# Optimization experiments

Hardware: AMD Instinct MI355X
Metric: run time of the kernel (lower is better)

Reference implementation:

```python
import jax, jax.numpy as jnp
import numpy as np

DIM, FFN, GC, NSET, K = 48, 2, 2, 32, 3
HID = DIM * FFN          # 96 hidden features
G = HID // GC            # 48 groups in KBA
CG = HID // G            # 2 channels per group
INTERC = 24              # min(dim, 24)
B, H, W = 4, 128, 128


def _conv(x, w, b=None, groups=1, pad=0):
    out = jax.lax.conv_general_dilated(
        x, w, (1, 1), [(pad, pad), (pad, pad)],
        dimension_numbers=('NCHW', 'OIHW', 'NCHW'),
        feature_group_count=groups)
    if b is not None:
        out = out + b[None, :, None, None]
    return out


def _kba(x, att, k, g, bb, ww):
    # x: [B,c,H,W], att: [B,nset,H,W], bb: [1,nset,c], ww: [1,nset,c*c//g*k*k]
    Bz, c, Hh, Ww = x.shape
    KK = k * k
    cg = c // g
    P = Hh * Ww
    a = att.reshape(Bz, -1, P).transpose(0, 2, 1)                     # [B,P,nset]
    bias = jnp.einsum('bpn,nc->bpc', a, bb[0])                        # [B,P,c]
    attk = jnp.einsum('bpn,nm->bpm', a, ww[0]).reshape(Bz, P, g, cg, cg * KK)
    pd = k // 2
    xp = jnp.pad(x, ((0, 0), (0, 0), (pd, pd), (pd, pd)))
    # im2col patches, torch.unfold layout: channel-major, kernel row-major
    patches = jnp.stack([xp[:, :, i:i + Hh, j:j + Ww]
                         for i in range(k) for j in range(k)], axis=2)  # [B,c,KK,H,W]
    uf = patches.reshape(Bz, g, cg * KK, P).transpose(0, 3, 1, 2)       # [B,P,g,cg*KK]
    out = jnp.einsum('bpgom,bpgm->bpgo', attk, uf).reshape(Bz, P, c) + bias
    return out.transpose(0, 2, 1).reshape(Bz, c, Hh, Ww)


def setup_inputs() -> dict:
    key = jax.random.key(0)
    ks = jax.random.split(key, 20)
    s = 0.05
    inp = {
        'x': jax.random.normal(ks[0], (B, DIM, H, W), jnp.float32),
        'dw1_w': jax.random.normal(ks[1], (HID, DIM, 1, 1), jnp.float32) * s,
        'dw2_w': jax.random.normal(ks[2], (HID, 1, 3, 3), jnp.float32) * s,
        'proj_w': jax.random.normal(ks[3], (DIM, HID, 1, 1), jnp.float32) * s,
        'sca_w': jax.random.normal(ks[4], (HID, HID, 1, 1), jnp.float32) * s,
        'sca_b': jax.random.normal(ks[5], (HID,), jnp.float32) * s,
        'c1_w1': jax.random.normal(ks[6], (HID, DIM, 1, 1), jnp.float32) * s,
        'c1_w2': jax.random.normal(ks[7], (HID, 1, 3, 3), jnp.float32) * s,
        'kba_w': jax.random.normal(ks[8], (1, NSET, HID * CG * K * K), jnp.float32) * s,
        'kba_b': jax.random.normal(ks[9], (1, NSET, HID), jnp.float32) * s,
        'c2_w1': jax.random.normal(ks[10], (INTERC, DIM // INTERC, 3, 3), jnp.float32) * s,
        'c2_b1': jax.random.normal(ks[11], (INTERC,), jnp.float32) * s,
        'c2_w2': jax.random.normal(ks[12], (NSET, INTERC // 2, 1, 1), jnp.float32) * s,
        'c2_b2': jax.random.normal(ks[13], (NSET,), jnp.float32) * s,
        'c211_w': jax.random.normal(ks[14], (NSET, DIM, 1, 1), jnp.float32) * s,
        'c211_b': jax.random.normal(ks[15], (NSET,), jnp.float32) * s,
        'attgamma': jnp.full((1, NSET, 1, 1), 0.01, jnp.float32),
        'ga1': jnp.full((1, HID, 1, 1), 0.01, jnp.float32),
    }
    return inp


def reference(x, dw1_w, dw2_w, proj_w, sca_w, sca_b, c1_w1, c1_w2,
              kba_w, kba_b, c2_w1, c2_b1, c2_w2, c2_b2,
              c211_w, c211_b, attgamma, ga1):
    # dwconv branch: 1x1 -> depthwise 3x3
    x1 = _conv(_conv(x, dw1_w), dw2_w, groups=HID, pad=1)
    # attention map branch: grouped 3x3 -> SimpleGate -> 1x1, scaled + skip 1x1
    t = _conv(x, c2_w1, c2_b1, groups=INTERC, pad=1)
    t1, t2 = jnp.split(t, 2, axis=1)
    t = _conv(t1 * t2, c2_w2, c2_b2)
    att = t * attgamma + _conv(x, c211_w, c211_b)
    # conv1 branch feeding KBA
    uf = _conv(_conv(x, c1_w1), c1_w2, groups=HID, pad=1)
    x2 = _kba(uf, att, K, G, kba_b, kba_w) * ga1 + uf
    comb = jax.nn.gelu(x1, approximate=False) * x2
    pooled = jnp.mean(comb, axis=(2, 3), keepdims=True)
    comb = comb * _conv(pooled, sca_w, sca_b)
    return _conv(comb, proj_w)
```

## Files before the change

### kernel.cpp

```cpp
#include <hip/hip_runtime.h>
#include <math.h>

#define BB 4
#define HH 128
#define WW 128
#define HWP (HH*WW)
#define DIMC 48
#define HIDC 96
#define NSETC 32

#define XS_W 27
#define HS_W 102
#define US_W 102

typedef __attribute__((ext_vector_type(8))) short bf16x8;
typedef __attribute__((ext_vector_type(4))) float f32x4;
typedef __attribute__((ext_vector_type(2))) float f32x2;

static __device__ __forceinline__ unsigned short f2bf(float f) {
    union { float f; unsigned u; } v; v.f = f;
    unsigned r = (v.u + 0x7FFFu + ((v.u >> 16) & 1u)) >> 16;
    return (unsigned short)r;
}
static __device__ __forceinline__ unsigned rnd_bf(float f) {
    union { float f; unsigned u; } v; v.f = f;
    return v.u + 0x8000u;
}
static __device__ __forceinline__ unsigned pack2bf(float lo, float hi) {
    return __builtin_amdgcn_perm(rnd_bf(hi), rnd_bf(lo), 0x07060302u);
}
static __device__ __forceinline__ void st_bf_hi(unsigned short* p, float f) {
    *p = (unsigned short)(rnd_bf(f) >> 16);
}
static __device__ __forceinline__ float bf2f(unsigned short u) {
    union { unsigned u; float f; } v; v.u = ((unsigned)u) << 16;
    return v.f;
}
static __device__ __forceinline__ float bfpair_lo(unsigned pr) {
    union { unsigned u; float f; } v; v.u = pr << 16; return v.f;
}
static __device__ __forceinline__ float bfpair_hi(unsigned pr) {
    union { unsigned u; float f; } v; v.u = pr & 0xffff0000u; return v.f;
}
static __device__ __forceinline__ float gelu(float x) {
    return 0.5f * x * (1.0f + erff(x * 0.70710678118654752f));
}

__global__ __launch_bounds__(256) void k_prep(
    const float* __restrict__ x,
    const float* __restrict__ kbaw, const float* __restrict__ kbab,
    const float* __restrict__ dw1w, const float* __restrict__ c1w1,
    const float* __restrict__ ga1,  const float* __restrict__ c211w,
    const float* __restrict__ c2w2, const float* __restrict__ c2b2,
    const float* __restrict__ c211b, const float* __restrict__ attg,
    unsigned short* __restrict__ Bpk, unsigned short* __restrict__ Bpw,
    unsigned short* __restrict__ Aps, unsigned short* __restrict__ Ag,
    unsigned* __restrict__ x_p, float* __restrict__ pooled)
{
    __shared__ unsigned ts[256 * 26];
    int blk = blockIdx.x, tid = threadIdx.x;
    if (blk < 300) {
        int t = blk * 256 + tid;
        if (t < 61440) {
            int j = t & 7, lane = (t >> 3) & 63, tile = t >> 9;
            int chunk = tile / 10, nt = tile - chunk * 10;
            int m = lane & 15, qn = lane >> 4;
            int lc = 4 * nt + (m & 3);
            int o = lc / 20, tt = lc % 20;
            int c = (m >> 2) * 24 + 2 * chunk + o;
            int n = qn * 8 + j;
            float v = 0.f;
            if (tt < 18)       v = kbaw[n * 1728 + (c >> 1) * 36 + (c & 1) * 18 + tt] * ga1[c];
            else if (tt == 18) v = kbab[n * 96 + c] * ga1[c];
            Bpk[t] = f2bf(v);
        } else if (t < 73728) {
            int u = t - 61440;
            int s = u / 6144;
            int rem = u % 6144;
            int nt = rem >> 9;
            int lane = (rem >> 3) & 63, j = rem & 7;
            int k = s * 32 + ((lane >> 4) << 3) + j;
            int col = (nt << 4) + (lane & 15);
            float v = 0.f;
            if (k < 48) v = (col < 96) ? dw1w[col * 48 + k] : c1w1[(col - 96) * 48 + k];
            Bpw[u] = f2bf(v);
        } else if (t < 75776) {
            int u = t - 73728;
            int j = u & 7, lane = (u >> 3) & 63, tile = u >> 9;
            int kt = tile >> 1, nt2 = tile & 1;
            int m = lane & 15, qn = lane >> 4;
            int n = 8 * (m >> 2) + 4 * nt2 + (m & 3);
            int k = kt * 32 + qn * 8 + j;
            Aps[u] = f2bf(k < 48 ? c211w[n * 48 + k] : 0.f);
        } else if (t < 76800) {
            int u = t - 75776;
            int j = u & 7, lane = (u >> 3) & 63, nt2 = u >> 9;
            int m = lane & 15, qn = lane >> 4;
            int n = 8 * (m >> 2) + 4 * nt2 + (m & 3);
            int k = qn * 8 + j;
            float v = 0.f;
            if (k < 12)       v = c2w2[n * 12 + k] * attg[n];
            else if (k == 12) v = c2b2[n] * attg[n] + c211b[n];
            Ag[u] = f2bf(v);
        }
    } else {
        int xblk = blk - 300;
        if (xblk == 0) {
            for (int i = tid; i < BB * HIDC; i += 256) pooled[i] = 0.f;
        }
        int b = xblk >> 6;
        int p0 = (xblk & 63) << 8;
        const float* xb = x + (size_t)b * DIMC * HWP + p0;
        #pragma unroll
        for (int c2 = 0; c2 < 24; ++c2) {
            float lo = xb[(2 * c2) * HWP + tid];
            float hi = xb[(2 * c2 + 1) * HWP + tid];
            ts[tid * 26 + c2] = pack2bf(lo, hi);
        }
        __syncthreads();
        unsigned* dst = x_p + ((size_t)b * HWP + p0) * 24;
        for (int idx = tid; idx < 256 * 24; idx += 256) {
            int px = idx / 24, j2 = idx - px * 24;
            dst[px * 24 + j2] = ts[px * 26 + j2];
        }
    }
}

__global__ __launch_bounds__(512, 4) void k_mff(
    const unsigned* __restrict__ x_p,
    const uint4* __restrict__ BpkA, const uint4* __restrict__ Bpw,
    const uint4* __restrict__ Aps,  const uint4* __restrict__ Ag,
    const float* __restrict__ c1w2, const float* __restrict__ dw2w,
    const float* __restrict__ c2w1, const float* __restrict__ c2b1,
    unsigned* __restrict__ comb_bf, float* __restrict__ pooled)
{
    __shared__ __attribute__((aligned(16))) unsigned xs[144 * XS_W];
    __shared__ __attribute__((aligned(16))) unsigned short hsw[144 * HS_W];
    __shared__ unsigned short us2p[100 * US_W];
    __shared__ float wls[864 + 432 + 24];
    __shared__ float pooled_s[96];

    int lane = threadIdx.x, wy = threadIdx.y;
    int tid = wy * 64 + lane;
    int blk = blockIdx.x;
    int b = blk >> 8, ty = (blk >> 4) & 15, tx = blk & 15;
    int q = lane >> 4, i16 = lane & 15;
    int wh = wy >> 2;
    int wp = wy & 3;

    float* wats  = wls + 864;
    float* c2b1s = wls + 864 + 432;
    float* att_tf = (float*)hsw;

    if (tid < 96) pooled_s[tid] = 0.f;
    for (int idx = tid; idx < 864; idx += 512) {
        int t5 = idx / 96, c = idx - t5 * 96;
        wls[idx] = dw2w[c * 9 + t5];
    }
    for (int idx = tid; idx < 216; idx += 512) {
        int g = idx / 9, tap = idx - g * 9;
        wats[idx * 2]     = c2w1[g * 18 + tap];
        wats[idx * 2 + 1] = c2w1[g * 18 + 9 + tap];
    }
    if (tid < 24) c2b1s[tid] = c2b1[tid];
    for (int idx = tid; idx < 144 * 12; idx += 512) {
        int pos = idx / 12, jp = idx - pos * 12;
        int gy = ty * 8 - 2 + pos / 12, gx = tx * 8 - 2 + pos % 12;
        uint2 v = {0u, 0u};
        if (((unsigned)gy < (unsigned)HH) & ((unsigned)gx < (unsigned)WW))
            v = *(const uint2*)&x_p[((size_t)b * HWP + gy * WW + gx) * 24 + jp * 2];
        xs[pos * XS_W + jp * 2]     = v.x;
        xs[pos * XS_W + jp * 2 + 1] = v.y;
    }
    __syncthreads();

    int p_t = wp * 16 + i16;
    int pyT = p_t >> 3, pxT = p_t & 7;
    int gp = (ty * 8 + pyT) * WW + tx * 8 + pxT;
    uint4 z4 = {0u, 0u, 0u, 0u};

    #pragma unroll
    for (int ci = 0; ci < 3; ++ci) {
        int g = q * 6 + wh * 3 + ci;
        float acc = c2b1s[g];
        #pragma unroll
        for (int di = 0; di < 3; ++di)
          #pragma unroll
          for (int dj = 0; dj < 3; ++dj) {
              unsigned pr = xs[((pyT + 1 + di) * 12 + pxT + 1 + dj) * XS_W + g];
              f32x2 w2 = *(const f32x2*)&wats[(g * 9 + di * 3 + dj) * 2];
              acc += w2.x * bfpair_lo(pr) + w2.y * bfpair_hi(pr);
          }
        att_tf[p_t * XS_W + g] = acc;
    }
    __syncthreads();

    bf16x8 afrag;
    {
        int p26 = p_t * XS_W;
        unsigned tgd[4];
        #pragma unroll
        for (int i2 = 0; i2 < 4; ++i2) {
            int k0 = q * 8 + 2 * i2;
            int k1 = k0 + 1;
            float v0 = (k0 < 12) ? att_tf[p26 + k0] * att_tf[p26 + 12 + k0] : (k0 == 12 ? 1.f : 0.f);
            float v1 = (k1 < 12) ? att_tf[p26 + k1] * att_tf[p26 + 12 + k1] : (k1 == 12 ? 1.f : 0.f);
            tgd[i2] = pack2bf(v0, v1);
        }
        uint4 tgr = {tgd[0], tgd[1], tgd[2], tgd[3]};
        bf16x8 btg = __builtin_bit_cast(bf16x8, tgr);

        int cen = (pyT + 2) * 12 + (pxT + 2);
        int cb = cen * XS_W + q * 4;
        uint4 bx0r = {xs[cb], xs[cb + 1], xs[cb + 2], xs[cb + 3]};
        uint4 bx1r = z4;
        if (q < 2) {
            int cb2 = cen * XS_W + 16 + q * 4;
            bx1r.x = xs[cb2]; bx1r.y = xs[cb2 + 1]; bx1r.z = xs[cb2 + 2]; bx1r.w = xs[cb2 + 3];
        }
        bf16x8 bx0 = __builtin_bit_cast(bf16x8, bx0r);
        bf16x8 bx1 = __builtin_bit_cast(bf16x8, bx1r);

        float attv[8];
        #pragma unroll
        for (int nt2 = 0; nt2 < 2; ++nt2) {
            bf16x8 ag  = __builtin_bit_cast(bf16x8, Ag[nt2 * 64 + lane]);
            bf16x8 as0 = __builtin_bit_cast(bf16x8, Aps[nt2 * 64 + lane]);
            bf16x8 as1 = __builtin_bit_cast(bf16x8, Aps[(2 + nt2) * 64 + lane]);
            f32x4 z = {0.f, 0.f, 0.f, 0.f};
            f32x4 c = __builtin_amdgcn_mfma_f32_16x16x32_bf16(ag, btg, z, 0, 0, 0);
            c = __builtin_amdgcn_mfma_f32_16x16x32_bf16(as1, bx1, c, 0, 0, 0);
            c = __builtin_amdgcn_mfma_f32_16x16x32_bf16(as0, bx0, c, 0, 0, 0);
            #pragma unroll
            for (int r = 0; r < 4; ++r) attv[nt2 * 4 + r] = c[r];
        }
        uint4 au = {pack2bf(attv[0], attv[1]), pack2bf(attv[2], attv[3]),
                    pack2bf(attv[4], attv[5]), pack2bf(attv[6], attv[7])};
        afrag = __builtin_bit_cast(bf16x8, au);
    }
    __syncthreads();

    {
        {
            int rg = wy;
            int hp = rg * 16 + i16;
            int ab = hp * XS_W + q * 4;
            uint4 a0r = {xs[ab], xs[ab + 1], xs[ab + 2], xs[ab + 3]};
            uint4 a1r = z4;
            if (q < 2) {
                int ab2 = hp * XS_W + 16 + q * 4;
                a1r.x = xs[ab2]; a1r.y = xs[ab2 + 1]; a1r.z = xs[ab2 + 2]; a1r.w = xs[ab2 + 3];
            }
            bf16x8 a0 = __builtin_bit_cast(bf16x8, a0r);
            bf16x8 a1 = __builtin_bit_cast(bf16x8, a1r);
            int rowb = rg * 16 + 4 * q;
            #pragma unroll
            for (int nt = 0; nt < 6; ++nt) {
                bf16x8 b0 = __builtin_bit_cast(bf16x8, Bpw[(size_t)((6 + nt) << 6) + lane]);
                bf16x8 b1 = __builtin_bit_cast(bf16x8, Bpw[(size_t)((18 + nt) << 6) + lane]);
                f32x4 z = {0.f, 0.f, 0.f, 0.f};
                f32x4 c = __builtin_amdgcn_mfma_f32_16x16x32_bf16(a1, b1, z, 0, 0, 0);
                c = __builtin_amdgcn_mfma_f32_16x16x32_bf16(a0, b0, c, 0, 0, 0);
                #pragma unroll
                for (int r = 0; r < 4; ++r)
                    st_bf_hi(&hsw[(rowb + r) * HS_W + nt * 16 + i16], c[r]);
            }
        }
        if (wy >= 1 && wy <= 6) {
            int hp = 128 + i16;
            int ab = hp * XS_W + q * 4;
            uint4 a0r = {xs[ab], xs[ab + 1], xs[ab + 2], xs[ab + 3]};
            uint4 a1r = z4;
            if (q < 2) {
                int ab2 = hp * XS_W + 16 + q * 4;
                a1r.x = xs[ab2]; a1r.y = xs[ab2 + 1]; a1r.z = xs[ab2 + 2]; a1r.w = xs[ab2 + 3];
            }
            bf16x8 a0 = __builtin_bit_cast(bf16x8, a0r);
            bf16x8 a1 = __builtin_bit_cast(bf16x8, a1r);
            int rowb = 128 + 4 * q;
            int nt = wy - 1;
            bf16x8 b0 = __builtin_bit_cast(bf16x8, Bpw[(size_t)((6 + nt) << 6) + lane]);
            bf16x8 b1 = __builtin_bit_cast(bf16x8, Bpw[(size_t)((18 + nt) << 6) + lane]);
            f32x4 z = {0.f, 0.f, 0.f, 0.f};
            f32x4 c = __builtin_amdgcn_mfma_f32_16x16x32_bf16(a1, b1, z, 0, 0, 0);
            c = __builtin_amdgcn_mfma_f32_16x16x32_bf16(a0, b0, c, 0, 0, 0);
            #pragma unroll
            for (int r = 0; r < 4; ++r)
                st_bf_hi(&hsw[(rowb + r) * HS_W + nt * 16 + i16], c[r]);
        }
    }
    __syncthreads();

    #pragma unroll 1
    for (int it = 0; it < 3; ++it) {
        int su = wy * 3 + it;
        int cq = su >> 1;
        const float* w9 = c1w2 + cq * 8 * 9;
        int hp2 = (su & 1) * 50 + lane;
        if (lane < 50) {
            int py2 = hp2 / 10, px2 = hp2 - py2 * 10;
            float acc[8];
            #pragma unroll
            for (int c = 0; c < 8; ++c) acc[c] = 0.f;
            #pragma unroll
            for (int di = 0; di < 3; ++di)
              #pragma unroll
              for (int dj = 0; dj < 3; ++dj) {
                  int rb = ((py2 + di) * 12 + px2 + dj) * HS_W + cq * 8;
                  unsigned pp[4];
                  pp[0] = *(const unsigned*)&hsw[rb];
                  pp[1] = *(const unsigned*)&hsw[rb + 2];
                  pp[2] = *(const unsigned*)&hsw[rb + 4];
                  pp[3] = *(const unsigned*)&hsw[rb + 6];
                  #pragma unroll
                  for (int c2 = 0; c2 < 4; ++c2) {
                      acc[2*c2]   += w9[(2*c2) * 9 + di * 3 + dj]   * bfpair_lo(pp[c2]);
                      acc[2*c2+1] += w9[(2*c2+1) * 9 + di * 3 + dj] * bfpair_hi(pp[c2]);
                  }
              }
            int wb = hp2 * US_W + cq * 8;
            *(unsigned*)&us2p[wb]     = pack2bf(acc[0], acc[1]);
            *(unsigned*)&us2p[wb + 2] = pack2bf(acc[2], acc[3]);
            *(unsigned*)&us2p[wb + 4] = pack2bf(acc[4], acc[5]);
            *(unsigned*)&us2p[wb + 6] = pack2bf(acc[6], acc[7]);
        }
    }
    __syncthreads();

    if (wy < 7) {
        int rg = wy;
        int hp = rg * 16 + i16;
        bool okp = hp < 100;
        int hy = hp / 10, hx = hp - hy * 10;
        int pos = okp ? ((hy + 1) * 12 + hx + 1) : 0;
        int ab = pos * XS_W + q * 4;
        uint4 a0r = {xs[ab], xs[ab + 1], xs[ab + 2], xs[ab + 3]};
        uint4 a1r = z4;
        if (q < 2) {
            int ab2 = pos * XS_W + 16 + q * 4;
            a1r.x = xs[ab2]; a1r.y = xs[ab2 + 1]; a1r.z = xs[ab2 + 2]; a1r.w = xs[ab2 + 3];
        }
        bf16x8 a0 = __builtin_bit_cast(bf16x8, a0r);
        bf16x8 a1 = __builtin_bit_cast(bf16x8, a1r);
        int rowb = rg * 16 + 4 * q;
        #pragma unroll
        for (int nt = 0; nt < 6; ++nt) {
            bf16x8 b0 = __builtin_bit_cast(bf16x8, Bpw[(size_t)(nt << 6) + lane]);
            bf16x8 b1 = __builtin_bit_cast(bf16x8, Bpw[(size_t)((12 + nt) << 6) + lane]);
            f32x4 z = {0.f, 0.f, 0.f, 0.f};
            f32x4 c = __builtin_amdgcn_mfma_f32_16x16x32_bf16(a1, b1, z, 0, 0, 0);
            c = __builtin_amdgcn_mfma_f32_16x16x32_bf16(a0, b0, c, 0, 0, 0);
            #pragma unroll
            for (int r = 0; r < 4; ++r)
                st_bf_hi(&hsw[(rowb + r) * HS_W + nt * 16 + i16], c[r]);
        }
    }
    __syncthreads();

    f32x2 greg[6];
    {
        int base = q * 24 + wh * 12;
        #pragma unroll
        for (int cc = 0; cc < 6; ++cc) {
            int c0 = base + 2 * cc;
            f32x2 acc = {0.f, 0.f};
            #pragma unroll
            for (int di = 0; di < 3; ++di)
              #pragma unroll
              for (int dj = 0; dj < 3; ++dj) {
                  unsigned pr = *(const unsigned*)&hsw[((pyT + di) * 10 + pxT + dj) * HS_W + c0];
                  f32x2 hv = {bfpair_lo(pr), bfpair_hi(pr)};
                  f32x2 wv = *(const f32x2*)&wls[(di * 3 + dj) * 96 + c0];
                  acc += wv * hv;
              }
            greg[cc].x = gelu(acc.x);
            greg[cc].y = gelu(acc.y);
        }
    }

    unsigned* cmb = comb_bf + ((size_t)b * HWP + gp) * 48 + q * 12;
    int hpC = (pyT + 1) * 10 + pxT + 1;
    const uint4* bpk_base = BpkA + (size_t)(wh * 60) * 64 + lane;

    uint4 buf[2][10];
    #pragma unroll
    for (int nt = 0; nt < 10; ++nt) buf[0][nt] = bpk_base[(size_t)nt << 6];

    #pragma unroll
    for (int cl = 0; cl < 6; ++cl) {
        int chunk = wh * 6 + cl;
        if (cl < 5) {
            #pragma unroll
            for (int nt = 0; nt < 10; ++nt)
                buf[(cl + 1) & 1][nt] = bpk_base[(size_t)(((cl + 1) * 10 + nt)) << 6];
        }
        int c0 = q * 24 + 2 * chunk;
        float u[18];
        #pragma unroll
        for (int i = 0; i < 3; ++i)
          #pragma unroll
          for (int j = 0; j < 3; ++j) {
              unsigned pr = *(const unsigned*)&us2p[((pyT + i) * 10 + pxT + j) * US_W + c0];
              u[i * 3 + j]     = bfpair_lo(pr);
              u[9 + i * 3 + j] = bfpair_hi(pr);
          }
        unsigned sp = *(const unsigned*)&us2p[hpC * US_W + c0];
        f32x4 cf[10];
        #pragma unroll
        for (int nt = 0; nt < 10; ++nt) {
            bf16x8 aW = __builtin_bit_cast(bf16x8, buf[cl & 1][nt]);
            f32x4 z = {0.f, 0.f, 0.f, 0.f};
            cf[nt] = __builtin_amdgcn_mfma_f32_16x16x32_bf16(aW, afrag, z, 0, 0, 0);
        }
        float acc0 = cf[4][2];
        float acc1 = cf[9][2];
        #pragma unroll
        for (int m = 0; m < 16; ++m) {
            acc0 += cf[m >> 2][m & 3]       * u[m];
            acc1 += cf[5 + (m >> 2)][m & 3] * u[m];
        }
        acc0 += cf[4][0] * u[16] + cf[4][1] * u[17];
        acc1 += cf[9][0] * u[16] + cf[9][1] * u[17];

        float x20 = acc0 + bfpair_lo(sp);
        float x21 = acc1 + bfpair_hi(sp);
        float cv0 = greg[cl].x * x20;
        float cv1 = greg[cl].y * x21;
        cmb[chunk] = pack2bf(cv0, cv1);
        float r0 = cv0, r1 = cv1;
        #pragma unroll
        for (int s = 1; s < 16; s <<= 1) {
            r0 += __shfl_xor(r0, s, 64);
            r1 += __shfl_xor(r1, s, 64);
        }
        if (i16 == 0) {
            atomicAdd(&pooled_s[c0], r0);
            atomicAdd(&pooled_s[c0 + 1], r1);
        }
    }
    __syncthreads();
    if (tid < 96) atomicAdd(&pooled[b * HIDC + tid], pooled_s[tid]);
}

__global__ __launch_bounds__(256) void k_final(
    const unsigned* __restrict__ comb_bf, const float* __restrict__ pooled,
    const float* __restrict__ scaw, const float* __restrict__ scab,
    const float* __restrict__ projw, float* __restrict__ out)
{
    __shared__ float svs[96];
    __shared__ float cs[96][66];
    int tid = threadIdx.x;
    int blk = blockIdx.x;
    int p0 = blk * 64;
    int b = p0 >> 14;
    if (tid < 96) {
        float dot = 0.f;
        const float* pr = pooled + b * 96;
        const float* wr = scaw + tid * 96;
        #pragma unroll 4
        for (int k = 0; k < 96; ++k) dot += wr[k] * pr[k];
        svs[tid] = scab[tid] + dot * (1.0f / (float)HWP);
    }
    __syncthreads();
    for (int idx = tid; idx < 64 * 12; idx += 256) {
        int px = idx / 12, cq = idx - px * 12;
        uint4 v = *(const uint4*)&comb_bf[(size_t)(p0 + px) * 48 + cq * 4];
        int k0 = cq * 8;
        unsigned pp[4] = {v.x, v.y, v.z, v.w};
        #pragma unroll
        for (int j = 0; j < 4; ++j) {
            cs[k0 + 2*j][px]     = bfpair_lo(pp[j]) * svs[k0 + 2*j];
            cs[k0 + 2*j + 1][px] = bfpair_hi(pp[j]) * svs[k0 + 2*j + 1];
        }
    }
    __syncthreads();
    int l = tid & 63, w = tid >> 6;
    int o0 = w * 12;
    float acc[12];
    #pragma unroll
    for (int o = 0; o < 12; ++o) acc[o] = 0.f;
    #pragma unroll 4
    for (int k = 0; k < 96; ++k) {
        float v = cs[k][l];
        #pragma unroll
        for (int o = 0; o < 12; ++o)
            acc[o] += projw[(o0 + o) * 96 + k] * v;
    }
    float* ob = out + (size_t)b * DIMC * HWP + (p0 & 16383) + l;
    #pragma unroll
    for (int o = 0; o < 12; ++o)
        ob[(o0 + o) * HWP] = acc[o];
}

extern "C" void kernel_launch(void* const* d_in, const int* in_sizes, int n_in,
                              void* d_out, int out_size, void* d_ws, size_t ws_size,
                              hipStream_t stream)
{
    const float* x     = (const float*)d_in[0];
    const float* dw1w  = (const float*)d_in[1];
    const float* dw2w  = (const float*)d_in[2];
    const float* projw = (const float*)d_in[3];
    const float* scaw  = (const float*)d_in[4];
    const float* scab  = (const float*)d_in[5];
    const float* c1w1  = (const float*)d_in[6];
    const float* c1w2  = (const float*)d_in[7];
    const float* kbaw  = (const float*)d_in[8];
    const float* kbab  = (const float*)d_in[9];
    const float* c2w1  = (const float*)d_in[10];
    const float* c2b1  = (const float*)d_in[11];
    const float* c2w2  = (const float*)d_in[12];
    const float* c2b2  = (const float*)d_in[13];
    const float* c211w = (const float*)d_in[14];
    const float* c211b = (const float*)d_in[15];
    const float* attg  = (const float*)d_in[16];
    const float* ga1   = (const float*)d_in[17];

    unsigned* x_p     = (unsigned*)d_ws;
    unsigned* comb_bf = x_p + (size_t)BB * HWP * 24;
    float* pooled     = (float*)(comb_bf + (size_t)BB * HWP * 48);
    unsigned short* BpkA = (unsigned short*)(pooled + BB * HIDC);
    unsigned short* Bpw  = BpkA + 61440;
    unsigned short* Aps  = Bpw + 12288;
    unsigned short* Ag   = Aps + 2048;

    k_prep <<<556,  256, 0, stream>>>(x, kbaw, kbab, dw1w, c1w1, ga1, c211w, c2w2, c2b2,
                                      c211b, attg, BpkA, Bpw, Aps, Ag, x_p, pooled);
    k_mff  <<<1024, dim3(64,8,1), 0, stream>>>(x_p, (const uint4*)BpkA, (const uint4*)Bpw,
                                               (const uint4*)Aps, (const uint4*)Ag,
                                               c1w2, dw2w, c2w1, c2b1, comb_bf, pooled);
    k_final<<<1024, 256, 0, stream>>>(comb_bf, pooled, scaw, scab, projw, (float*)d_out);
}
```

Measured before the change: 212.9 us.

## Stage conv1 depthwise weights in LDS, vectorize FMAs, drop B-fragment double buffering

New measurement: 196.7 us. 1.08x faster.

```diff
diff --git a/kernel.cpp b/kernel.cpp
--- a/kernel.cpp
+++ b/kernel.cpp
@@ -31,10 +31,6 @@
 }
 static __device__ __forceinline__ void st_bf_hi(unsigned short* p, float f) {
     *p = (unsigned short)(rnd_bf(f) >> 16);
-}
-static __device__ __forceinline__ float bf2f(unsigned short u) {
-    union { unsigned u; float f; } v; v.u = ((unsigned)u) << 16;
-    return v.f;
 }
 static __device__ __forceinline__ float bfpair_lo(unsigned pr) {
     union { unsigned u; float f; } v; v.u = pr << 16; return v.f;
@@ -126,7 +122,7 @@
     }
 }
 
-__global__ __launch_bounds__(512, 4) void k_mff(
+__global__ __launch_bounds__(512, 2) void k_mff(
     const unsigned* __restrict__ x_p,
     const uint4* __restrict__ BpkA, const uint4* __restrict__ Bpw,
     const uint4* __restrict__ Aps,  const uint4* __restrict__ Ag,
@@ -136,8 +132,9 @@
 {
     __shared__ __attribute__((aligned(16))) unsigned xs[144 * XS_W];
     __shared__ __attribute__((aligned(16))) unsigned short hsw[144 * HS_W];
-    __shared__ unsigned short us2p[100 * US_W];
-    __shared__ float wls[864 + 432 + 24];
+    __shared__ __attribute__((aligned(16))) unsigned short us2p[100 * US_W];
+    __shared__ __attribute__((aligned(16))) float wls[864 + 432 + 24];
+    __shared__ __attribute__((aligned(16))) float c1s[864];
     __shared__ float pooled_s[96];
 
     int lane = threadIdx.x, wy = threadIdx.y;
@@ -156,6 +153,7 @@
     for (int idx = tid; idx < 864; idx += 512) {
         int t5 = idx / 96, c = idx - t5 * 96;
         wls[idx] = dw2w[c * 9 + t5];
+        c1s[idx] = c1w2[c * 9 + t5];
     }
     for (int idx = tid; idx < 216; idx += 512) {
         int g = idx / 9, tap = idx - g * 9;
@@ -182,16 +180,17 @@
     #pragma unroll
     for (int ci = 0; ci < 3; ++ci) {
         int g = q * 6 + wh * 3 + ci;
-        float acc = c2b1s[g];
+        f32x2 av = {0.f, 0.f};
         #pragma unroll
         for (int di = 0; di < 3; ++di)
           #pragma unroll
           for (int dj = 0; dj < 3; ++dj) {
               unsigned pr = xs[((pyT + 1 + di) * 12 + pxT + 1 + dj) * XS_W + g];
               f32x2 w2 = *(const f32x2*)&wats[(g * 9 + di * 3 + dj) * 2];
-              acc += w2.x * bfpair_lo(pr) + w2.y * bfpair_hi(pr);
+              f32x2 hv = {bfpair_lo(pr), bfpair_hi(pr)};
+              av += w2 * hv;
           }
-        att_tf[p_t * XS_W + g] = acc;
+        att_tf[p_t * XS_W + g] = c2b1s[g] + av.x + av.y;
     }
     __syncthreads();
 
@@ -295,13 +294,12 @@
     for (int it = 0; it < 3; ++it) {
         int su = wy * 3 + it;
         int cq = su >> 1;
-        const float* w9 = c1w2 + cq * 8 * 9;
         int hp2 = (su & 1) * 50 + lane;
         if (lane < 50) {
             int py2 = hp2 / 10, px2 = hp2 - py2 * 10;
-            float acc[8];
-            #pragma unroll
-            for (int c = 0; c < 8; ++c) acc[c] = 0.f;
+            f32x2 a2[4];
+            #pragma unroll
+            for (int c = 0; c < 4; ++c) a2[c] = (f32x2){0.f, 0.f};
             #pragma unroll
             for (int di = 0; di < 3; ++di)
               #pragma unroll
@@ -312,17 +310,18 @@
                   pp[1] = *(const unsigned*)&hsw[rb + 2];
                   pp[2] = *(const unsigned*)&hsw[rb + 4];
                   pp[3] = *(const unsigned*)&hsw[rb + 6];
+                  const f32x2* wrow = (const f32x2*)&c1s[(di * 3 + dj) * 96 + cq * 8];
                   #pragma unroll
                   for (int c2 = 0; c2 < 4; ++c2) {
-                      acc[2*c2]   += w9[(2*c2) * 9 + di * 3 + dj]   * bfpair_lo(pp[c2]);
-                      acc[2*c2+1] += w9[(2*c2+1) * 9 + di * 3 + dj] * bfpair_hi(pp[c2]);
+                      f32x2 hv = {bfpair_lo(pp[c2]), bfpair_hi(pp[c2])};
+                      a2[c2] += wrow[c2] * hv;
                   }
               }
             int wb = hp2 * US_W + cq * 8;
-            *(unsigned*)&us2p[wb]     = pack2bf(acc[0], acc[1]);
-            *(unsigned*)&us2p[wb + 2] = pack2bf(acc[2], acc[3]);
-            *(unsigned*)&us2p[wb + 4] = pack2bf(acc[4], acc[5]);
-            *(unsigned*)&us2p[wb + 6] = pack2bf(acc[6], acc[7]);
+            *(unsigned*)&us2p[wb]     = pack2bf(a2[0].x, a2[0].y);
+            *(unsigned*)&us2p[wb + 2] = pack2bf(a2[1].x, a2[1].y);
+            *(unsigned*)&us2p[wb + 4] = pack2bf(a2[2].x, a2[2].y);
+            *(unsigned*)&us2p[wb + 6] = pack2bf(a2[3].x, a2[3].y);
         }
     }
     __syncthreads();
@@ -379,21 +378,10 @@
     }
 
     unsigned* cmb = comb_bf + ((size_t)b * HWP + gp) * 48 + q * 12;
-    int hpC = (pyT + 1) * 10 + pxT + 1;
-    const uint4* bpk_base = BpkA + (size_t)(wh * 60) * 64 + lane;
-
-    uint4 buf[2][10];
-    #pragma unroll
-    for (int nt = 0; nt < 10; ++nt) buf[0][nt] = bpk_base[(size_t)nt << 6];
 
     #pragma unroll
     for (int cl = 0; cl < 6; ++cl) {
         int chunk = wh * 6 + cl;
-        if (cl < 5) {
-            #pragma unroll
-            for (int nt = 0; nt < 10; ++nt)
-                buf[(cl + 1) & 1][nt] = bpk_base[(size_t)(((cl + 1) * 10 + nt)) << 6];
-        }
         int c0 = q * 24 + 2 * chunk;
         float u[18];
         #pragma unroll
@@ -404,26 +392,30 @@
               u[i * 3 + j]     = bfpair_lo(pr);
               u[9 + i * 3 + j] = bfpair_hi(pr);
           }
-        unsigned sp = *(const unsigned*)&us2p[hpC * US_W + c0];
         f32x4 cf[10];
         #pragma unroll
         for (int nt = 0; nt < 10; ++nt) {
-            bf16x8 aW = __builtin_bit_cast(bf16x8, buf[cl & 1][nt]);
+            bf16x8 aW = __builtin_bit_cast(bf16x8, BpkA[(size_t)((chunk * 10 + nt) << 6) + lane]);
             f32x4 z = {0.f, 0.f, 0.f, 0.f};
             cf[nt] = __builtin_amdgcn_mfma_f32_16x16x32_bf16(aW, afrag, z, 0, 0, 0);
         }
-        float acc0 = cf[4][2];
-        float acc1 = cf[9][2];
-        #pragma unroll
-        for (int m = 0; m < 16; ++m) {
-            acc0 += cf[m >> 2][m & 3]       * u[m];
-            acc1 += cf[5 + (m >> 2)][m & 3] * u[m];
-        }
-        acc0 += cf[4][0] * u[16] + cf[4][1] * u[17];
-        acc1 += cf[9][0] * u[16] + cf[9][1] * u[17];
-
-        float x20 = acc0 + bfpair_lo(sp);
-        float x21 = acc1 + bfpair_hi(sp);
+        float s0a = cf[4][2], s1a = cf[9][2];
+        float s0b = 0.f,      s1b = 0.f;
+        #pragma unroll
+        for (int m = 0; m < 8; ++m) {
+            s0a += cf[m >> 2][m & 3]       * u[m];
+            s1a += cf[5 + (m >> 2)][m & 3] * u[m];
+        }
+        #pragma unroll
+        for (int m = 8; m < 16; ++m) {
+            s0b += cf[m >> 2][m & 3]       * u[m];
+            s1b += cf[5 + (m >> 2)][m & 3] * u[m];
+        }
+        s0b += cf[4][0] * u[16] + cf[4][1] * u[17];
+        s1b += cf[9][0] * u[16] + cf[9][1] * u[17];
+
+        float x20 = (s0a + s0b) + u[4];
+        float x21 = (s1a + s1b) + u[13];
         float cv0 = greg[cl].x * x20;
         float cv1 = greg[cl].y * x21;
         cmb[chunk] = pack2bf(cv0, cv1);
```
